# Optimization experiments

Measured on AMD Instinct MI355X. Metric: run time of the kernel, lower is better.

## Reference

```python
import jax, jax.numpy as jnp
import numpy as np

N = 100000
E = 1600000
NFEAT = 128
NHID = 128
NCLASS = 10


def setup_inputs() -> dict:
    key = jax.random.key(0)
    ks = jax.random.split(key, 12)
    x = jax.random.normal(ks[0], (N, NFEAT), dtype=jnp.float32)
    edge_index = jax.random.randint(ks[1], (2, E), 0, N, dtype=jnp.int64)
    s = 0.05
    W1 = jax.random.normal(ks[2], (NFEAT, NHID), dtype=jnp.float32) * s
    b1 = jnp.zeros((NHID,), dtype=jnp.float32)
    W2 = jax.random.normal(ks[3], (NHID, NHID), dtype=jnp.float32) * s
    b2 = jnp.zeros((NHID,), dtype=jnp.float32)
    W3 = jax.random.normal(ks[4], (NHID, NHID), dtype=jnp.float32) * s
    b3 = jnp.zeros((NHID,), dtype=jnp.float32)
    Wl = jax.random.normal(ks[5], (NHID, NCLASS), dtype=jnp.float32) * s
    bl = jnp.zeros((NCLASS,), dtype=jnp.float32)
    return {"x": x, "edge_index": edge_index, "W1": W1, "b1": b1,
            "W2": W2, "b2": b2, "W3": W3, "b3": b3, "Wl": Wl, "bl": bl}


def _gcn_norm(edge_index, num_nodes):
    # PyG gcn_norm with add_self_loops=True and unit edge weights.
    loops = jnp.arange(num_nodes, dtype=edge_index.dtype)
    src = jnp.concatenate([edge_index[0], loops])  # [E+N]
    dst = jnp.concatenate([edge_index[1], loops])
    ones = jnp.ones(src.shape[0], dtype=jnp.float32)
    deg = jax.ops.segment_sum(ones, dst, num_segments=num_nodes)
    dis = jax.lax.rsqrt(deg)  # deg >= 1 due to self-loops
    norm = dis[src] * dis[dst]  # [E+N]
    return src, dst, norm


def _gcn_conv(h, src, dst, norm, W, b, num_nodes):
    h = h @ W                                   # [N, out]
    msg = h[src] * norm[:, None]                # gather + edge scaling
    out = jax.ops.segment_sum(msg, dst, num_segments=num_nodes)
    return out + b


def reference(x, edge_index, W1, b1, W2, b2, W3, b3, Wl, bl):
    src, dst, norm = _gcn_norm(edge_index, N)
    h = jax.nn.relu(_gcn_conv(x, src, dst, norm, W1, b1, N))
    h = jax.nn.relu(_gcn_conv(h, src, dst, norm, W2, b2, N))
    h = _gcn_conv(h, src, dst, norm, W3, b3, N)
    logits = h @ Wl + bl                        # dropout is identity (eval / p=0)
    return jax.nn.log_softmax(logits, axis=1)
```

## Files before the change

### kernel.cpp

```cpp
#include <hip/hip_runtime.h>

#define NFEAT 128
#define NCLS  10
#define NCP   16
#define BROW  512
#define BINC  4096

static inline size_t alignup(size_t x) { return (x + 255) & ~size_t(255); }

__device__ __forceinline__ ushort f2bf(float f) {
  uint x = __float_as_uint(f);
  return (ushort)((x + 0x7fffu + ((x >> 16) & 1u)) >> 16);
}
__device__ __forceinline__ float bf2f(ushort u) {
  return __uint_as_float(((uint)u) << 16);
}

typedef short bf16x8 __attribute__((ext_vector_type(8)));
typedef float f32x4 __attribute__((ext_vector_type(4)));


__global__ void zero_ints(int* __restrict__ p, int n) {
  int i = blockIdx.x * 256 + threadIdx.x;
  if (i < n) p[i] = 0;
}

__global__ __launch_bounds__(256) void bucket_hist(const int* __restrict__ dst,
                                                   int* __restrict__ bkt_cnt,
                                                   int e, int nbkt) {
  __shared__ int hist[256];
  for (int t = threadIdx.x; t < nbkt; t += 256) hist[t] = 0;
  __syncthreads();
  int i = blockIdx.x * 256 + threadIdx.x;
  int stride = gridDim.x * 256;
  for (; i < e; i += stride) atomicAdd(&hist[dst[i] >> 9], 1);
  __syncthreads();
  for (int t = threadIdx.x; t < nbkt; t += 256)
    if (hist[t]) atomicAdd(&bkt_cnt[t], hist[t]);
}

__global__ __launch_bounds__(256) void bkt_scan(const int* __restrict__ bkt_cnt,
                                                int* __restrict__ bkt_off,
                                                int* __restrict__ gfrontier,
                                                int n, int nbkt) {
  __shared__ int sbuf[256];
  const int t = threadIdx.x;
  int x = 0;
  if (t < nbkt) {
    int lo = t << 9;
    int nodes = n - lo; if (nodes > BROW) nodes = BROW;
    x = bkt_cnt[t] + nodes;
  }
  sbuf[t] = x;
  __syncthreads();
  for (int off = 1; off < 256; off <<= 1) {
    int v = (t >= off) ? sbuf[t - off] : 0;
    __syncthreads();
    sbuf[t] += v;
    __syncthreads();
  }
  if (t < nbkt) { bkt_off[t] = sbuf[t] - x; gfrontier[t] = sbuf[t] - x; }
  if (t == nbkt - 1) bkt_off[nbkt] = sbuf[t];
}

__global__ __launch_bounds__(256) void bin_items(const int* __restrict__ ei,
                                                 int nE, int total, int nbkt,
                                                 int* __restrict__ gfrontier,
                                                 int2* __restrict__ binned) {
  __shared__ int hist[256];
  __shared__ int loff[256];
  __shared__ int gbase[256];
  __shared__ int sbuf[256];
  __shared__ int2 st[BINC];
  const int t = threadIdx.x;
  const int chunk0 = blockIdx.x * BINC;
  for (int q = t; q < nbkt; q += 256) hist[q] = 0;
  __syncthreads();
  for (int j = t; j < BINC; j += 256) {
    int i = chunk0 + j;
    if (i < total) {
      int d = (i < nE) ? ei[nE + i] : (i - nE);
      atomicAdd(&hist[d >> 9], 1);
    }
  }
  __syncthreads();
  int x = (t < nbkt) ? hist[t] : 0;
  sbuf[t] = x;
  __syncthreads();
  for (int off = 1; off < 256; off <<= 1) {
    int v = (t >= off) ? sbuf[t - off] : 0;
    __syncthreads();
    sbuf[t] += v;
    __syncthreads();
  }
  loff[t] = sbuf[t] - x;
  gbase[t] = (t < nbkt && x > 0) ? atomicAdd(&gfrontier[t], x) : 0;
  __syncthreads();
  hist[t] = loff[t];
  __syncthreads();
  for (int j = t; j < BINC; j += 256) {
    int i = chunk0 + j;
    if (i < total) {
      int s, d;
      if (i < nE) { s = ei[i]; d = ei[nE + i]; }
      else        { s = i - nE; d = s; }
      int p = atomicAdd(&hist[d >> 9], 1);
      st[p] = make_int2(s, d);
    }
  }
  __syncthreads();
  int M = total - chunk0; if (M > BINC) M = BINC;
  for (int j = t; j < M; j += 256) {
    int2 it = st[j];
    int b = it.y >> 9;
    binned[gbase[b] + (j - loff[b])] = it;
  }
}

__global__ __launch_bounds__(512) void bucket_finalize(const int2* __restrict__ binned,
                                                       const int* __restrict__ bkt_off,
                                                       int* __restrict__ row_ptr,
                                                       float* __restrict__ dis,
                                                       int* __restrict__ ev,
                                                       int n, int nbkt) {
  __shared__ int hist[BROW];
  __shared__ int sbuf[BROW];
  __shared__ int pre[BROW];
  __shared__ int front[BROW];
  const int b = blockIdx.x;
  const int t = threadIdx.x;
  const int row0 = b << 9;
  const int beg = bkt_off[b], end = bkt_off[b + 1];
  hist[t] = 0; front[t] = 0;
  __syncthreads();
  for (int j = beg + t; j < end; j += BROW)
    atomicAdd(&hist[binned[j].y - row0], 1);
  __syncthreads();
  const int x = hist[t];
  const int v = row0 + t;
  if (v < n) dis[v] = rsqrtf((float)x);
  sbuf[t] = x;
  __syncthreads();
  for (int off = 1; off < BROW; off <<= 1) {
    int val = (t >= off) ? sbuf[t - off] : 0;
    __syncthreads();
    sbuf[t] += val;
    __syncthreads();
  }
  pre[t] = sbuf[t] - x;
  if (v < n) row_ptr[v] = beg + pre[t];
  if (b == nbkt - 1 && t == 0) row_ptr[n] = end;
  __syncthreads();
  for (int j = beg + t; j < end; j += BROW) {
    int2 it = binned[j];
    int dl = it.y - row0;
    int slot = atomicAdd(&front[dl], 1);
    ev[beg + pre[dl] + slot] = it.x;
  }
}


__global__ __launch_bounds__(256) void fold_weights(const float* __restrict__ W3,
                                                    const float* __restrict__ Wl,
                                                    const float* __restrict__ b3,
                                                    const float* __restrict__ bl,
                                                    float* __restrict__ Wf,
                                                    float* __restrict__ bf) {
  int t = blockIdx.x * blockDim.x + threadIdx.x;
  if (t < NFEAT * NCP) {
    int r = t >> 4, c = t & 15;
    float s = 0.f;
    if (c < NCLS) {
      for (int k = 0; k < NFEAT; ++k) s += W3[r * NFEAT + k] * Wl[k * NCLS + c];
    }
    Wf[t] = s;
  }
  if (t < NCP) {
    float s = 0.f;
    if (t < NCLS) {
      s = bl[t];
      for (int k = 0; k < NFEAT; ++k) s += b3[k] * Wl[k * NCLS + t];
    }
    bf[t] = s;
  }
}

__global__ __launch_bounds__(256) void prep_w(const float* __restrict__ W,
                                              ushort* __restrict__ Wt) {
  int t = blockIdx.x * 256 + threadIdx.x;
  if (t < NFEAT * NFEAT) {
    int n = t >> 7, k = t & 127;
    Wt[n * NFEAT + k] = f2bf(W[k * NFEAT + n]);
  }
}


__global__ __launch_bounds__(256) void gemm_mfma(const float* __restrict__ A,
                                                 const ushort* __restrict__ Wt,
                                                 const float* __restrict__ dis,
                                                 ushort* __restrict__ Cb, int nrows) {
  __shared__ __align__(16) ushort As[64 * NFEAT];
  const int tid = threadIdx.x;
  const int row0 = blockIdx.x * 64;
  {
    const int m = tid >> 2;
    const int kc = (tid & 3) * 32;
    const int gr = row0 + m;
    float4 f[8];
    if (gr < nrows) {
      #pragma unroll
      for (int q = 0; q < 8; ++q)
        f[q] = *(const float4*)&A[(size_t)gr * NFEAT + kc + q * 4];
    } else {
      #pragma unroll
      for (int q = 0; q < 8; ++q) f[q] = make_float4(0.f, 0.f, 0.f, 0.f);
    }
    #pragma unroll
    for (int q = 0; q < 4; ++q) {
      union { ushort u[8]; int4 v; } pk;
      const float* fp = (const float*)&f[q * 2];
      #pragma unroll
      for (int j = 0; j < 8; ++j) pk.u[j] = f2bf(fp[j]);
      int byte = (m * 256 + (kc + q * 8) * 2) ^ ((m & 7) << 4);
      *(int4*)((char*)As + byte) = pk.v;
    }
  }
  __syncthreads();
  const int wave = tid >> 6;
  const int lane = tid & 63;
  const int m0 = wave * 16;
  bf16x8 afr[4];
  #pragma unroll
  for (int ks = 0; ks < 4; ++ks) {
    int m = m0 + (lane & 15);
    int kk = ks * 32 + (lane >> 4) * 8;
    int byte = (m * 256 + kk * 2) ^ ((m & 7) << 4);
    afr[ks] = *(const bf16x8*)((const char*)As + byte);
  }
  f32x4 acc[8];
  #pragma unroll
  for (int c = 0; c < 8; ++c) acc[c] = (f32x4){0.f, 0.f, 0.f, 0.f};
  #pragma unroll
  for (int c = 0; c < 8; ++c) {
    #pragma unroll
    for (int ks = 0; ks < 4; ++ks) {
      int n = c * 16 + (lane & 15);
      int kk = ks * 32 + (lane >> 4) * 8;
      bf16x8 bfr = *(const bf16x8*)&Wt[n * NFEAT + kk];
      acc[c] = __builtin_amdgcn_mfma_f32_16x16x32_bf16(afr[ks], bfr, acc[c], 0, 0, 0);
    }
  }
  const int gr_base = row0 + m0 + (lane >> 4) * 4;
  float dr[4];
  #pragma unroll
  for (int r = 0; r < 4; ++r)
    dr[r] = (gr_base + r < nrows) ? dis[gr_base + r] : 0.f;
  #pragma unroll
  for (int c = 0; c < 8; ++c) {
    #pragma unroll
    for (int r = 0; r < 4; ++r) {
      int gr = gr_base + r;
      if (gr < nrows)
        Cb[(size_t)gr * NFEAT + c * 16 + (lane & 15)] = f2bf(acc[c][r] * dr[r]);
    }
  }
}


__global__ __launch_bounds__(256) void aggregate(const ushort* __restrict__ hw,
                                                 const int* __restrict__ row_ptr,
                                                 const int* __restrict__ ev,
                                                 const float* __restrict__ dis,
                                                 const float* __restrict__ bias,
                                                 float* __restrict__ out,
                                                 int relu, int n) {
  const int wave = threadIdx.x >> 6;
  const int lane = threadIdx.x & 63;
  const int v = blockIdx.x * 4 + wave;
  if (v >= n) return;
  const int beg = row_ptr[v], end = row_ptr[v + 1];
  const int half = lane >> 5;
  const int hl = lane & 31;
  float4 acc = make_float4(0.f, 0.f, 0.f, 0.f);
  int e = beg + half;
  for (; e + 6 < end; e += 8) {
    int s0 = ev[e];
    int s1 = ev[e + 2];
    int s2 = ev[e + 4];
    int s3 = ev[e + 6];
    ushort4 q0 = *(const ushort4*)&hw[(size_t)s0 * NFEAT + hl * 4];
    ushort4 q1 = *(const ushort4*)&hw[(size_t)s1 * NFEAT + hl * 4];
    ushort4 q2 = *(const ushort4*)&hw[(size_t)s2 * NFEAT + hl * 4];
    ushort4 q3 = *(const ushort4*)&hw[(size_t)s3 * NFEAT + hl * 4];
    acc.x += bf2f(q0.x) + bf2f(q1.x) + bf2f(q2.x) + bf2f(q3.x);
    acc.y += bf2f(q0.y) + bf2f(q1.y) + bf2f(q2.y) + bf2f(q3.y);
    acc.z += bf2f(q0.z) + bf2f(q1.z) + bf2f(q2.z) + bf2f(q3.z);
    acc.w += bf2f(q0.w) + bf2f(q1.w) + bf2f(q2.w) + bf2f(q3.w);
  }
  for (; e < end; e += 2) {
    int s = ev[e];
    ushort4 q = *(const ushort4*)&hw[(size_t)s * NFEAT + hl * 4];
    acc.x += bf2f(q.x); acc.y += bf2f(q.y);
    acc.z += bf2f(q.z); acc.w += bf2f(q.w);
  }
  acc.x += __shfl_xor(acc.x, 32);
  acc.y += __shfl_xor(acc.y, 32);
  acc.z += __shfl_xor(acc.z, 32);
  acc.w += __shfl_xor(acc.w, 32);
  if (half == 0) {
    float dv = dis[v];
    float4 b = *(const float4*)&bias[hl * 4];
    acc.x = acc.x * dv + b.x; acc.y = acc.y * dv + b.y;
    acc.z = acc.z * dv + b.z; acc.w = acc.w * dv + b.w;
    if (relu) {
      acc.x = fmaxf(acc.x, 0.f); acc.y = fmaxf(acc.y, 0.f);
      acc.z = fmaxf(acc.z, 0.f); acc.w = fmaxf(acc.w, 0.f);
    }
    *(float4*)&out[(size_t)v * NFEAT + hl * 4] = acc;
  }
}


__global__ __launch_bounds__(256) void gemm_small(const float* __restrict__ A,
                                                  const float* __restrict__ Wf,
                                                  const float* __restrict__ dis,
                                                  float* __restrict__ G, int n) {
  __shared__ float Ws[NFEAT * NCP];
  for (int i = threadIdx.x; i < NFEAT * NCP; i += 256) Ws[i] = Wf[i];
  __syncthreads();
  const int v = blockIdx.x * 256 + threadIdx.x;
  if (v >= n) return;
  const float* Arow = A + (size_t)v * NFEAT;
  float acc[NCP];
  #pragma unroll
  for (int c = 0; c < NCP; ++c) acc[c] = 0.f;
  #pragma unroll 4
  for (int k = 0; k < NFEAT; k += 4) {
    float4 a = *(const float4*)&Arow[k];
    float av[4] = {a.x, a.y, a.z, a.w};
    #pragma unroll
    for (int j = 0; j < 4; ++j) {
      #pragma unroll
      for (int cq = 0; cq < NCP; cq += 4) {
        float4 w = *(const float4*)&Ws[(k + j) * NCP + cq];
        acc[cq + 0] += av[j] * w.x;
        acc[cq + 1] += av[j] * w.y;
        acc[cq + 2] += av[j] * w.z;
        acc[cq + 3] += av[j] * w.w;
      }
    }
  }
  const float dv = dis[v];
  #pragma unroll
  for (int cq = 0; cq < NCP; cq += 4)
    *(float4*)&G[(size_t)v * NCP + cq] =
        make_float4(acc[cq] * dv, acc[cq + 1] * dv, acc[cq + 2] * dv, acc[cq + 3] * dv);
}


__global__ __launch_bounds__(256) void agg_logits(const float* __restrict__ G,
                                                  const int* __restrict__ row_ptr,
                                                  const int* __restrict__ ev,
                                                  const float* __restrict__ dis,
                                                  const float* __restrict__ bf,
                                                  float* __restrict__ out, int n) {
  const int wave = threadIdx.x >> 6;
  const int lane = threadIdx.x & 63;
  const int v = blockIdx.x * 4 + wave;
  if (v >= n) return;
  const int beg = row_ptr[v], end = row_ptr[v + 1];
  const int g = lane >> 4;
  const int f = lane & 15;
  float acc = 0.f;
  int e = beg + g;
  for (; e + 4 < end; e += 8) {
    int s0 = ev[e];
    int s1 = ev[e + 4];
    acc += G[(size_t)s0 * NCP + f] + G[(size_t)s1 * NCP + f];
  }
  for (; e < end; e += 4) {
    acc += G[(size_t)ev[e] * NCP + f];
  }
  acc += __shfl_xor(acc, 16);
  acc += __shfl_xor(acc, 32);
  float logit = dis[v] * acc + bf[f];
  float pv = (f < NCLS) ? logit : -INFINITY;
  float m = pv;
  #pragma unroll
  for (int s = 8; s >= 1; s >>= 1) m = fmaxf(m, __shfl_xor(m, s));
  float ex = (f < NCLS) ? expf(logit - m) : 0.f;
  float ssum = ex;
  #pragma unroll
  for (int s = 8; s >= 1; s >>= 1) ssum += __shfl_xor(ssum, s);
  float lse = m + logf(ssum);
  if (g == 0 && f < NCLS) out[(size_t)v * NCLS + f] = logit - lse;
}


extern "C" void kernel_launch(void* const* d_in, const int* in_sizes, int n_in,
                              void* d_out, int out_size, void* d_ws, size_t ws_size,
                              hipStream_t stream) {
  const float* x  = (const float*)d_in[0];
  const int*   ei = (const int*)d_in[1];
  const float* W1 = (const float*)d_in[2];
  const float* b1 = (const float*)d_in[3];
  const float* W2 = (const float*)d_in[4];
  const float* b2 = (const float*)d_in[5];
  const float* W3 = (const float*)d_in[6];
  const float* b3 = (const float*)d_in[7];
  const float* Wl = (const float*)d_in[8];
  const float* bl = (const float*)d_in[9];
  float* out = (float*)d_out;

  const int nN = in_sizes[0] / NFEAT;
  const int nE = in_sizes[1] / 2;
  const int total = nN + nE;
  const int nbkt = (nN + BROW - 1) >> 9;
  const int nbBin = (total + BINC - 1) / BINC;

  char* ws = (char*)d_ws;
  int*    bkt_cnt = (int*)ws;     ws += alignup(256 * 4);
  int*    bkt_off = (int*)ws;     ws += alignup(257 * 4);
  int*    gfront  = (int*)ws;     ws += alignup(256 * 4);
  int*    row_ptr = (int*)ws;     ws += alignup((size_t)(nN + 1) * 4);
  float*  dis     = (float*)ws;   ws += alignup((size_t)nN * 4);
  float*  Wf      = (float*)ws;   ws += alignup((size_t)NFEAT * NCP * 4);
  float*  bf      = (float*)ws;   ws += alignup((size_t)NCP * 4);
  ushort* Wt1     = (ushort*)ws;  ws += alignup((size_t)NFEAT * NFEAT * 2);
  ushort* Wt2     = (ushort*)ws;  ws += alignup((size_t)NFEAT * NFEAT * 2);
  int2*   binned  = (int2*)ws;    ws += alignup((size_t)total * 8);
  int*    ev      = (int*)ws;     ws += alignup((size_t)total * 4);
  ushort* hb      = (ushort*)ws;  ws += alignup((size_t)nN * NFEAT * 2);
  float*  bufA    = (float*)ws;   ws += alignup((size_t)nN * NFEAT * 4);
  float*  G       = (float*)ws;   ws += alignup((size_t)nN * NCP * 4);

  zero_ints<<<1, 256, 0, stream>>>(bkt_cnt, nbkt);
  bucket_hist<<<512, 256, 0, stream>>>(ei + nE, bkt_cnt, nE, nbkt);
  bkt_scan<<<1, 256, 0, stream>>>(bkt_cnt, bkt_off, gfront, nN, nbkt);
  bin_items<<<nbBin, 256, 0, stream>>>(ei, nE, total, nbkt, gfront, binned);
  bucket_finalize<<<nbkt, BROW, 0, stream>>>(binned, bkt_off, row_ptr, dis, ev, nN, nbkt);

  fold_weights<<<8, 256, 0, stream>>>(W3, Wl, b3, bl, Wf, bf);
  prep_w<<<64, 256, 0, stream>>>(W1, Wt1);
  prep_w<<<64, 256, 0, stream>>>(W2, Wt2);

  const int gemm_grid = (nN + 63) / 64;
  const int node_grid = (nN + 3) / 4;

  gemm_mfma<<<gemm_grid, 256, 0, stream>>>(x, Wt1, dis, hb, nN);
  aggregate<<<node_grid, 256, 0, stream>>>(hb, row_ptr, ev, dis, b1, bufA, 1, nN);
  gemm_mfma<<<gemm_grid, 256, 0, stream>>>(bufA, Wt2, dis, hb, nN);
  aggregate<<<node_grid, 256, 0, stream>>>(hb, row_ptr, ev, dis, b2, bufA, 1, nN);
  gemm_small<<<(nN + 255) / 256, 256, 0, stream>>>(bufA, Wf, dis, G, nN);
  agg_logits<<<node_grid, 256, 0, stream>>>(G, row_ptr, ev, dis, bf, out, nN);
}
```

Baseline: 359.7 us.

## Store hidden features as feature-sliced bf16 planes to shrink gather working set

Hidden activations are stored as 8 planes of 16 features each (bf16) instead of row-major 128-wide rows. Each aggregate block works on one plane for 16 nodes, so the random gather touches a 3.2 MB plane that can stay cache-resident instead of the full feature matrix. Aggregate outputs are also written as bf16 planes rather than fp32, which halves the intermediate traffic feeding the next GEMM. The cost is that each edge list is re-read 8 times and each gathered access is only 8 bytes, and the GEMMs need plane-strided loads and stores.

```diff
diff --git a/kernel.cpp b/kernel.cpp
--- a/kernel.cpp
+++ b/kernel.cpp
@@ -195,34 +195,56 @@
 }
 
 
+template<bool SLICED>
 __global__ __launch_bounds__(256) void gemm_mfma(const float* __restrict__ A,
+                                                 const ushort* __restrict__ AS,
+                                                 size_t pstride,
                                                  const ushort* __restrict__ Wt,
                                                  const float* __restrict__ dis,
-                                                 ushort* __restrict__ Cb, int nrows) {
-  __shared__ __align__(16) ushort As[64 * NFEAT];
+                                                 ushort* __restrict__ CbS, int nrows) {
+  __shared__ __align__(16) ushort Asm[64 * NFEAT];
   const int tid = threadIdx.x;
   const int row0 = blockIdx.x * 64;
   {
     const int m = tid >> 2;
     const int kc = (tid & 3) * 32;
     const int gr = row0 + m;
-    float4 f[8];
-    if (gr < nrows) {
+    int4 u[4];
+    if (SLICED) {
+      if (gr < nrows) {
+        const int p0 = kc >> 4;
+        const ushort* pl0 = AS + (size_t)p0 * pstride + (size_t)gr * 16;
+        const ushort* pl1 = pl0 + pstride;
+        u[0] = *(const int4*)pl0;
+        u[1] = *(const int4*)(pl0 + 8);
+        u[2] = *(const int4*)pl1;
+        u[3] = *(const int4*)(pl1 + 8);
+      } else {
+        u[0] = u[1] = u[2] = u[3] = make_int4(0, 0, 0, 0);
+      }
+    } else {
+      float4 f[8];
+      if (gr < nrows) {
+        #pragma unroll
+        for (int q = 0; q < 8; ++q)
+          f[q] = *(const float4*)&A[(size_t)gr * NFEAT + kc + q * 4];
+      } else {
+        #pragma unroll
+        for (int q = 0; q < 8; ++q) f[q] = make_float4(0.f, 0.f, 0.f, 0.f);
+      }
       #pragma unroll
-      for (int q = 0; q < 8; ++q)
-        f[q] = *(const float4*)&A[(size_t)gr * NFEAT + kc + q * 4];
-    } else {
-      #pragma unroll
-      for (int q = 0; q < 8; ++q) f[q] = make_float4(0.f, 0.f, 0.f, 0.f);
+      for (int q = 0; q < 4; ++q) {
+        union { ushort us[8]; int4 v; } pk;
+        const float* fp = (const float*)&f[q * 2];
+        #pragma unroll
+        for (int j = 0; j < 8; ++j) pk.us[j] = f2bf(fp[j]);
+        u[q] = pk.v;
+      }
     }
     #pragma unroll
     for (int q = 0; q < 4; ++q) {
-      union { ushort u[8]; int4 v; } pk;
-      const float* fp = (const float*)&f[q * 2];
-      #pragma unroll
-      for (int j = 0; j < 8; ++j) pk.u[j] = f2bf(fp[j]);
       int byte = (m * 256 + (kc + q * 8) * 2) ^ ((m & 7) << 4);
-      *(int4*)((char*)As + byte) = pk.v;
+      *(int4*)((char*)Asm + byte) = u[q];
     }
   }
   __syncthreads();
@@ -235,7 +257,7 @@
     int m = m0 + (lane & 15);
     int kk = ks * 32 + (lane >> 4) * 8;
     int byte = (m * 256 + kk * 2) ^ ((m & 7) << 4);
-    afr[ks] = *(const bf16x8*)((const char*)As + byte);
+    afr[ks] = *(const bf16x8*)((const char*)Asm + byte);
   }
   f32x4 acc[8];
   #pragma unroll
@@ -257,71 +279,74 @@
     dr[r] = (gr_base + r < nrows) ? dis[gr_base + r] : 0.f;
   #pragma unroll
   for (int c = 0; c < 8; ++c) {
+    ushort* plane = CbS + (size_t)c * pstride;
     #pragma unroll
     for (int r = 0; r < 4; ++r) {
       int gr = gr_base + r;
       if (gr < nrows)
-        Cb[(size_t)gr * NFEAT + c * 16 + (lane & 15)] = f2bf(acc[c][r] * dr[r]);
-    }
-  }
-}
-
-
-__global__ __launch_bounds__(256) void aggregate(const ushort* __restrict__ hw,
+        plane[(size_t)gr * 16 + (lane & 15)] = f2bf(acc[c][r] * dr[r]);
+    }
+  }
+}
+
+
+__global__ __launch_bounds__(256) void aggregate(const ushort* __restrict__ hbS,
                                                  const int* __restrict__ row_ptr,
                                                  const int* __restrict__ ev,
                                                  const float* __restrict__ dis,
                                                  const float* __restrict__ bias,
-                                                 float* __restrict__ out,
-                                                 int relu, int n) {
+                                                 ushort* __restrict__ outS,
+                                                 size_t pstride, int relu, int n) {
+  const int s = blockIdx.x & 7;
+  const int chunk = blockIdx.x >> 3;
   const int wave = threadIdx.x >> 6;
   const int lane = threadIdx.x & 63;
-  const int v = blockIdx.x * 4 + wave;
-  if (v >= n) return;
-  const int beg = row_ptr[v], end = row_ptr[v + 1];
-  const int half = lane >> 5;
-  const int hl = lane & 31;
-  float4 acc = make_float4(0.f, 0.f, 0.f, 0.f);
-  int e = beg + half;
-  for (; e + 6 < end; e += 8) {
-    int s0 = ev[e];
-    int s1 = ev[e + 2];
-    int s2 = ev[e + 4];
-    int s3 = ev[e + 6];
-    ushort4 q0 = *(const ushort4*)&hw[(size_t)s0 * NFEAT + hl * 4];
-    ushort4 q1 = *(const ushort4*)&hw[(size_t)s1 * NFEAT + hl * 4];
-    ushort4 q2 = *(const ushort4*)&hw[(size_t)s2 * NFEAT + hl * 4];
-    ushort4 q3 = *(const ushort4*)&hw[(size_t)s3 * NFEAT + hl * 4];
-    acc.x += bf2f(q0.x) + bf2f(q1.x) + bf2f(q2.x) + bf2f(q3.x);
-    acc.y += bf2f(q0.y) + bf2f(q1.y) + bf2f(q2.y) + bf2f(q3.y);
-    acc.z += bf2f(q0.z) + bf2f(q1.z) + bf2f(q2.z) + bf2f(q3.z);
-    acc.w += bf2f(q0.w) + bf2f(q1.w) + bf2f(q2.w) + bf2f(q3.w);
-  }
-  for (; e < end; e += 2) {
-    int s = ev[e];
-    ushort4 q = *(const ushort4*)&hw[(size_t)s * NFEAT + hl * 4];
-    acc.x += bf2f(q.x); acc.y += bf2f(q.y);
-    acc.z += bf2f(q.z); acc.w += bf2f(q.w);
-  }
-  acc.x += __shfl_xor(acc.x, 32);
-  acc.y += __shfl_xor(acc.y, 32);
-  acc.z += __shfl_xor(acc.z, 32);
-  acc.w += __shfl_xor(acc.w, 32);
-  if (half == 0) {
-    float dv = dis[v];
-    float4 b = *(const float4*)&bias[hl * 4];
-    acc.x = acc.x * dv + b.x; acc.y = acc.y * dv + b.y;
-    acc.z = acc.z * dv + b.z; acc.w = acc.w * dv + b.w;
-    if (relu) {
-      acc.x = fmaxf(acc.x, 0.f); acc.y = fmaxf(acc.y, 0.f);
-      acc.z = fmaxf(acc.z, 0.f); acc.w = fmaxf(acc.w, 0.f);
-    }
-    *(float4*)&out[(size_t)v * NFEAT + hl * 4] = acc;
-  }
-}
-
-
-__global__ __launch_bounds__(256) void gemm_small(const float* __restrict__ A,
+  const int f4 = lane & 3;
+  const int ep = lane >> 2;
+  const ushort* plane = hbS + (size_t)s * pstride;
+  ushort* oplane = outS + (size_t)s * pstride;
+  const float4 bs = *(const float4*)&bias[s * 16 + f4 * 4];
+  #pragma unroll
+  for (int q = 0; q < 4; ++q) {
+    const int v = chunk * 16 + wave * 4 + q;
+    if (v >= n) return;
+    const int beg = row_ptr[v], end = row_ptr[v + 1];
+    float4 acc = make_float4(0.f, 0.f, 0.f, 0.f);
+    for (int e = beg + ep; e < end; e += 16) {
+      int src = __builtin_nontemporal_load(&ev[e]);
+      ushort4 q4 = *(const ushort4*)&plane[(size_t)src * 16 + f4 * 4];
+      acc.x += bf2f(q4.x); acc.y += bf2f(q4.y);
+      acc.z += bf2f(q4.z); acc.w += bf2f(q4.w);
+    }
+    #pragma unroll
+    for (int off = 4; off <= 32; off <<= 1) {
+      acc.x += __shfl_xor(acc.x, off);
+      acc.y += __shfl_xor(acc.y, off);
+      acc.z += __shfl_xor(acc.z, off);
+      acc.w += __shfl_xor(acc.w, off);
+    }
+    if (ep == 0) {
+      const float dv = dis[v];
+      float4 r;
+      r.x = fmaf(acc.x, dv, bs.x);
+      r.y = fmaf(acc.y, dv, bs.y);
+      r.z = fmaf(acc.z, dv, bs.z);
+      r.w = fmaf(acc.w, dv, bs.w);
+      if (relu) {
+        r.x = fmaxf(r.x, 0.f); r.y = fmaxf(r.y, 0.f);
+        r.z = fmaxf(r.z, 0.f); r.w = fmaxf(r.w, 0.f);
+      }
+      union { ushort us[4]; uint2 q2; } pk;
+      pk.us[0] = f2bf(r.x); pk.us[1] = f2bf(r.y);
+      pk.us[2] = f2bf(r.z); pk.us[3] = f2bf(r.w);
+      *(uint2*)&oplane[(size_t)v * 16 + f4 * 4] = pk.q2;
+    }
+  }
+}
+
+
+__global__ __launch_bounds__(256) void gemm_small(const ushort* __restrict__ AS,
+                                                  size_t pstride,
                                                   const float* __restrict__ Wf,
                                                   const float* __restrict__ dis,
                                                   float* __restrict__ G, int n) {
@@ -330,23 +355,26 @@
   __syncthreads();
   const int v = blockIdx.x * 256 + threadIdx.x;
   if (v >= n) return;
-  const float* Arow = A + (size_t)v * NFEAT;
   float acc[NCP];
   #pragma unroll
   for (int c = 0; c < NCP; ++c) acc[c] = 0.f;
-  #pragma unroll 4
-  for (int k = 0; k < NFEAT; k += 4) {
-    float4 a = *(const float4*)&Arow[k];
-    float av[4] = {a.x, a.y, a.z, a.w};
+  #pragma unroll
+  for (int p = 0; p < 8; ++p) {
+    union { ushort us[16]; int4 q[2]; } a;
+    const ushort* pl = AS + (size_t)p * pstride + (size_t)v * 16;
+    a.q[0] = *(const int4*)pl;
+    a.q[1] = *(const int4*)(pl + 8);
     #pragma unroll
-    for (int j = 0; j < 4; ++j) {
+    for (int j = 0; j < 16; ++j) {
+      float av = bf2f(a.us[j]);
+      int k = p * 16 + j;
       #pragma unroll
       for (int cq = 0; cq < NCP; cq += 4) {
-        float4 w = *(const float4*)&Ws[(k + j) * NCP + cq];
-        acc[cq + 0] += av[j] * w.x;
-        acc[cq + 1] += av[j] * w.y;
-        acc[cq + 2] += av[j] * w.z;
-        acc[cq + 3] += av[j] * w.w;
+        float4 w = *(const float4*)&Ws[k * NCP + cq];
+        acc[cq + 0] += av * w.x;
+        acc[cq + 1] += av * w.y;
+        acc[cq + 2] += av * w.z;
+        acc[cq + 3] += av * w.w;
       }
     }
   }
@@ -417,6 +445,7 @@
   const int total = nN + nE;
   const int nbkt = (nN + BROW - 1) >> 9;
   const int nbBin = (total + BINC - 1) / BINC;
+  const size_t pstride = (size_t)nN * 16;
 
   char* ws = (char*)d_ws;
   int*    bkt_cnt = (int*)ws;     ws += alignup(256 * 4);
@@ -425,13 +454,13 @@
   int*    row_ptr = (int*)ws;     ws += alignup((size_t)(nN + 1) * 4);
   float*  dis     = (float*)ws;   ws += alignup((size_t)nN * 4);
   float*  Wf      = (float*)ws;   ws += alignup((size_t)NFEAT * NCP * 4);
-  float*  bf      = (float*)ws;   ws += alignup((size_t)NCP * 4);
+  float*  bfv     = (float*)ws;   ws += alignup((size_t)NCP * 4);
   ushort* Wt1     = (ushort*)ws;  ws += alignup((size_t)NFEAT * NFEAT * 2);
   ushort* Wt2     = (ushort*)ws;  ws += alignup((size_t)NFEAT * NFEAT * 2);
   int2*   binned  = (int2*)ws;    ws += alignup((size_t)total * 8);
   int*    ev      = (int*)ws;     ws += alignup((size_t)total * 4);
-  ushort* hb      = (ushort*)ws;  ws += alignup((size_t)nN * NFEAT * 2);
-  float*  bufA    = (float*)ws;   ws += alignup((size_t)nN * NFEAT * 4);
+  ushort* hbS     = (ushort*)ws;  ws += alignup((size_t)nN * NFEAT * 2);
+  ushort* aggS    = (ushort*)ws;  ws += alignup((size_t)nN * NFEAT * 2);
   float*  G       = (float*)ws;   ws += alignup((size_t)nN * NCP * 4);
 
   zero_ints<<<1, 256, 0, stream>>>(bkt_cnt, nbkt);
@@ -440,17 +469,18 @@
   bin_items<<<nbBin, 256, 0, stream>>>(ei, nE, total, nbkt, gfront, binned);
   bucket_finalize<<<nbkt, BROW, 0, stream>>>(binned, bkt_off, row_ptr, dis, ev, nN, nbkt);
 
-  fold_weights<<<8, 256, 0, stream>>>(W3, Wl, b3, bl, Wf, bf);
+  fold_weights<<<8, 256, 0, stream>>>(W3, Wl, b3, bl, Wf, bfv);
   prep_w<<<64, 256, 0, stream>>>(W1, Wt1);
   prep_w<<<64, 256, 0, stream>>>(W2, Wt2);
 
   const int gemm_grid = (nN + 63) / 64;
+  const int agg_grid = ((nN + 15) / 16) * 8;
   const int node_grid = (nN + 3) / 4;
 
-  gemm_mfma<<<gemm_grid, 256, 0, stream>>>(x, Wt1, dis, hb, nN);
-  aggregate<<<node_grid, 256, 0, stream>>>(hb, row_ptr, ev, dis, b1, bufA, 1, nN);
-  gemm_mfma<<<gemm_grid, 256, 0, stream>>>(bufA, Wt2, dis, hb, nN);
-  aggregate<<<node_grid, 256, 0, stream>>>(hb, row_ptr, ev, dis, b2, bufA, 1, nN);
-  gemm_small<<<(nN + 255) / 256, 256, 0, stream>>>(bufA, Wf, dis, G, nN);
-  agg_logits<<<node_grid, 256, 0, stream>>>(G, row_ptr, ev, dis, bf, out, nN);
-}
+  gemm_mfma<false><<<gemm_grid, 256, 0, stream>>>(x, nullptr, pstride, Wt1, dis, hbS, nN);
+  aggregate<<<agg_grid, 256, 0, stream>>>(hbS, row_ptr, ev, dis, b1, aggS, pstride, 1, nN);
+  gemm_mfma<true><<<gemm_grid, 256, 0, stream>>>(nullptr, aggS, pstride, Wt2, dis, hbS, nN);
+  aggregate<<<agg_grid, 256, 0, stream>>>(hbS, row_ptr, ev, dis, b2, aggS, pstride, 1, nN);
+  gemm_small<<<(nN + 255) / 256, 256, 0, stream>>>(aggS, pstride, Wf, dis, G, nN);
+  agg_logits<<<node_grid, 256, 0, stream>>>(G, row_ptr, ev, dis, bfv, out, nN);
+}
```

Measured after the change: 710.6 us. 1.98x slower.

## Fuse aggregation with following GEMM via shared-memory tile and bf16 intermediates

Applied to the files above, without the earlier changes.

Each aggregation step now writes its ReLU'd 64-row tile into shared memory as bf16 and immediately runs the next MFMA GEMM, so the fp32 intermediate buffer is never written to or re-read from global memory. The folded W3·Wl projection now runs on MFMA with a single 16-column tile, and the logits intermediate G is stored as bf16. Small launches are also merged: a memset replaces the zero kernel and the two weight preps become one kernel. The risks are lower occupancy, since each block aggregates 16 nodes per wave serially before the GEMM, and extra bf16 rounding of intermediates.

```diff
diff --git a/kernel.cpp b/kernel.cpp
--- a/kernel.cpp
+++ b/kernel.cpp
@@ -19,11 +19,6 @@
 typedef short bf16x8 __attribute__((ext_vector_type(8)));
 typedef float f32x4 __attribute__((ext_vector_type(4)));
 
-
-__global__ void zero_ints(int* __restrict__ p, int n) {
-  int i = blockIdx.x * 256 + threadIdx.x;
-  if (i < n) p[i] = 0;
-}
 
 __global__ __launch_bounds__(256) void bucket_hist(const int* __restrict__ dst,
                                                    int* __restrict__ bkt_cnt,
@@ -164,7 +159,7 @@
                                                     const float* __restrict__ Wl,
                                                     const float* __restrict__ b3,
                                                     const float* __restrict__ bl,
-                                                    float* __restrict__ Wf,
+                                                    ushort* __restrict__ Wft,
                                                     float* __restrict__ bf) {
   int t = blockIdx.x * blockDim.x + threadIdx.x;
   if (t < NFEAT * NCP) {
@@ -173,7 +168,7 @@
     if (c < NCLS) {
       for (int k = 0; k < NFEAT; ++k) s += W3[r * NFEAT + k] * Wl[k * NCLS + c];
     }
-    Wf[t] = s;
+    Wft[c * NFEAT + r] = f2bf(s);
   }
   if (t < NCP) {
     float s = 0.f;
@@ -185,13 +180,15 @@
   }
 }
 
-__global__ __launch_bounds__(256) void prep_w(const float* __restrict__ W,
-                                              ushort* __restrict__ Wt) {
+__global__ __launch_bounds__(256) void prep_w2(const float* __restrict__ W1,
+                                               const float* __restrict__ W2,
+                                               ushort* __restrict__ Wt1,
+                                               ushort* __restrict__ Wt2) {
   int t = blockIdx.x * 256 + threadIdx.x;
-  if (t < NFEAT * NFEAT) {
-    int n = t >> 7, k = t & 127;
-    Wt[n * NFEAT + k] = f2bf(W[k * NFEAT + n]);
-  }
+  int u = t & 16383;
+  int n = u >> 7, k = u & 127;
+  if (t < 16384) Wt1[n * NFEAT + k] = f2bf(W1[k * NFEAT + n]);
+  else           Wt2[n * NFEAT + k] = f2bf(W2[k * NFEAT + n]);
 }
 
 
@@ -199,7 +196,7 @@
                                                  const ushort* __restrict__ Wt,
                                                  const float* __restrict__ dis,
                                                  ushort* __restrict__ Cb, int nrows) {
-  __shared__ __align__(16) ushort As[64 * NFEAT];
+  __shared__ __align__(16) ushort Asm[64 * NFEAT];
   const int tid = threadIdx.x;
   const int row0 = blockIdx.x * 64;
   {
@@ -217,12 +214,12 @@
     }
     #pragma unroll
     for (int q = 0; q < 4; ++q) {
-      union { ushort u[8]; int4 v; } pk;
+      union { ushort us[8]; int4 v; } pk;
       const float* fp = (const float*)&f[q * 2];
       #pragma unroll
-      for (int j = 0; j < 8; ++j) pk.u[j] = f2bf(fp[j]);
+      for (int j = 0; j < 8; ++j) pk.us[j] = f2bf(fp[j]);
       int byte = (m * 256 + (kc + q * 8) * 2) ^ ((m & 7) << 4);
-      *(int4*)((char*)As + byte) = pk.v;
+      *(int4*)((char*)Asm + byte) = pk.v;
     }
   }
   __syncthreads();
@@ -235,7 +232,7 @@
     int m = m0 + (lane & 15);
     int kk = ks * 32 + (lane >> 4) * 8;
     int byte = (m * 256 + kk * 2) ^ ((m & 7) << 4);
-    afr[ks] = *(const bf16x8*)((const char*)As + byte);
+    afr[ks] = *(const bf16x8*)((const char*)Asm + byte);
   }
   f32x4 acc[8];
   #pragma unroll
@@ -267,98 +264,111 @@
 }
 
 
-__global__ __launch_bounds__(256) void aggregate(const ushort* __restrict__ hw,
-                                                 const int* __restrict__ row_ptr,
-                                                 const int* __restrict__ ev,
-                                                 const float* __restrict__ dis,
-                                                 const float* __restrict__ bias,
-                                                 float* __restrict__ out,
-                                                 int relu, int n) {
-  const int wave = threadIdx.x >> 6;
-  const int lane = threadIdx.x & 63;
-  const int v = blockIdx.x * 4 + wave;
-  if (v >= n) return;
-  const int beg = row_ptr[v], end = row_ptr[v + 1];
+template<int NCT>
+__global__ __launch_bounds__(256) void fused_agg_gemm(const ushort* __restrict__ hw,
+                                                      const int* __restrict__ row_ptr,
+                                                      const int* __restrict__ ev,
+                                                      const float* __restrict__ dis,
+                                                      const float* __restrict__ bias,
+                                                      const ushort* __restrict__ Wt,
+                                                      ushort* __restrict__ outB, int n) {
+  __shared__ __align__(16) ushort Hs[64 * NFEAT];
+  const int tid = threadIdx.x;
+  const int wave = tid >> 6;
+  const int lane = tid & 63;
   const int half = lane >> 5;
   const int hl = lane & 31;
-  float4 acc = make_float4(0.f, 0.f, 0.f, 0.f);
-  int e = beg + half;
-  for (; e + 6 < end; e += 8) {
-    int s0 = ev[e];
-    int s1 = ev[e + 2];
-    int s2 = ev[e + 4];
-    int s3 = ev[e + 6];
-    ushort4 q0 = *(const ushort4*)&hw[(size_t)s0 * NFEAT + hl * 4];
-    ushort4 q1 = *(const ushort4*)&hw[(size_t)s1 * NFEAT + hl * 4];
-    ushort4 q2 = *(const ushort4*)&hw[(size_t)s2 * NFEAT + hl * 4];
-    ushort4 q3 = *(const ushort4*)&hw[(size_t)s3 * NFEAT + hl * 4];
-    acc.x += bf2f(q0.x) + bf2f(q1.x) + bf2f(q2.x) + bf2f(q3.x);
-    acc.y += bf2f(q0.y) + bf2f(q1.y) + bf2f(q2.y) + bf2f(q3.y);
-    acc.z += bf2f(q0.z) + bf2f(q1.z) + bf2f(q2.z) + bf2f(q3.z);
-    acc.w += bf2f(q0.w) + bf2f(q1.w) + bf2f(q2.w) + bf2f(q3.w);
-  }
-  for (; e < end; e += 2) {
-    int s = ev[e];
-    ushort4 q = *(const ushort4*)&hw[(size_t)s * NFEAT + hl * 4];
-    acc.x += bf2f(q.x); acc.y += bf2f(q.y);
-    acc.z += bf2f(q.z); acc.w += bf2f(q.w);
-  }
-  acc.x += __shfl_xor(acc.x, 32);
-  acc.y += __shfl_xor(acc.y, 32);
-  acc.z += __shfl_xor(acc.z, 32);
-  acc.w += __shfl_xor(acc.w, 32);
-  if (half == 0) {
-    float dv = dis[v];
-    float4 b = *(const float4*)&bias[hl * 4];
-    acc.x = acc.x * dv + b.x; acc.y = acc.y * dv + b.y;
-    acc.z = acc.z * dv + b.z; acc.w = acc.w * dv + b.w;
-    if (relu) {
-      acc.x = fmaxf(acc.x, 0.f); acc.y = fmaxf(acc.y, 0.f);
-      acc.z = fmaxf(acc.z, 0.f); acc.w = fmaxf(acc.w, 0.f);
-    }
-    *(float4*)&out[(size_t)v * NFEAT + hl * 4] = acc;
-  }
-}
-
-
-__global__ __launch_bounds__(256) void gemm_small(const float* __restrict__ A,
-                                                  const float* __restrict__ Wf,
-                                                  const float* __restrict__ dis,
-                                                  float* __restrict__ G, int n) {
-  __shared__ float Ws[NFEAT * NCP];
-  for (int i = threadIdx.x; i < NFEAT * NCP; i += 256) Ws[i] = Wf[i];
-  __syncthreads();
-  const int v = blockIdx.x * 256 + threadIdx.x;
-  if (v >= n) return;
-  const float* Arow = A + (size_t)v * NFEAT;
-  float acc[NCP];
-  #pragma unroll
-  for (int c = 0; c < NCP; ++c) acc[c] = 0.f;
-  #pragma unroll 4
-  for (int k = 0; k < NFEAT; k += 4) {
-    float4 a = *(const float4*)&Arow[k];
-    float av[4] = {a.x, a.y, a.z, a.w};
+  const int row0 = blockIdx.x * 64;
+  const float4 bs = *(const float4*)&bias[hl * 4];
+  for (int q = 0; q < 16; ++q) {
+    const int m = wave * 16 + q;
+    const int v = row0 + m;
+    float4 acc = make_float4(0.f, 0.f, 0.f, 0.f);
+    if (v < n) {
+      const int beg = row_ptr[v], end = row_ptr[v + 1];
+      int e = beg + half;
+      for (; e + 6 < end; e += 8) {
+        int s0 = ev[e];
+        int s1 = ev[e + 2];
+        int s2 = ev[e + 4];
+        int s3 = ev[e + 6];
+        ushort4 q0 = *(const ushort4*)&hw[(size_t)s0 * NFEAT + hl * 4];
+        ushort4 q1 = *(const ushort4*)&hw[(size_t)s1 * NFEAT + hl * 4];
+        ushort4 q2 = *(const ushort4*)&hw[(size_t)s2 * NFEAT + hl * 4];
+        ushort4 q3 = *(const ushort4*)&hw[(size_t)s3 * NFEAT + hl * 4];
+        acc.x += bf2f(q0.x) + bf2f(q1.x) + bf2f(q2.x) + bf2f(q3.x);
+        acc.y += bf2f(q0.y) + bf2f(q1.y) + bf2f(q2.y) + bf2f(q3.y);
+        acc.z += bf2f(q0.z) + bf2f(q1.z) + bf2f(q2.z) + bf2f(q3.z);
+        acc.w += bf2f(q0.w) + bf2f(q1.w) + bf2f(q2.w) + bf2f(q3.w);
+      }
+      for (; e < end; e += 2) {
+        int s = ev[e];
+        ushort4 q4 = *(const ushort4*)&hw[(size_t)s * NFEAT + hl * 4];
+        acc.x += bf2f(q4.x); acc.y += bf2f(q4.y);
+        acc.z += bf2f(q4.z); acc.w += bf2f(q4.w);
+      }
+      acc.x += __shfl_xor(acc.x, 32);
+      acc.y += __shfl_xor(acc.y, 32);
+      acc.z += __shfl_xor(acc.z, 32);
+      acc.w += __shfl_xor(acc.w, 32);
+    }
+    if (half == 0) {
+      float r0 = 0.f, r1 = 0.f, r2 = 0.f, r3 = 0.f;
+      if (v < n) {
+        const float dv = dis[v];
+        r0 = fmaxf(fmaf(acc.x, dv, bs.x), 0.f);
+        r1 = fmaxf(fmaf(acc.y, dv, bs.y), 0.f);
+        r2 = fmaxf(fmaf(acc.z, dv, bs.z), 0.f);
+        r3 = fmaxf(fmaf(acc.w, dv, bs.w), 0.f);
+      }
+      union { ushort us[4]; uint2 q2; } pk;
+      pk.us[0] = f2bf(r0); pk.us[1] = f2bf(r1);
+      pk.us[2] = f2bf(r2); pk.us[3] = f2bf(r3);
+      int byte = (m * 256 + hl * 8) ^ ((m & 7) << 4);
+      *(uint2*)((char*)Hs + byte) = pk.q2;
+    }
+  }
+  __syncthreads();
+  const int m0 = wave * 16;
+  bf16x8 afr[4];
+  #pragma unroll
+  for (int ks = 0; ks < 4; ++ks) {
+    int m = m0 + (lane & 15);
+    int kk = ks * 32 + (lane >> 4) * 8;
+    int byte = (m * 256 + kk * 2) ^ ((m & 7) << 4);
+    afr[ks] = *(const bf16x8*)((const char*)Hs + byte);
+  }
+  f32x4 acc[NCT];
+  #pragma unroll
+  for (int c = 0; c < NCT; ++c) acc[c] = (f32x4){0.f, 0.f, 0.f, 0.f};
+  #pragma unroll
+  for (int c = 0; c < NCT; ++c) {
     #pragma unroll
-    for (int j = 0; j < 4; ++j) {
-      #pragma unroll
-      for (int cq = 0; cq < NCP; cq += 4) {
-        float4 w = *(const float4*)&Ws[(k + j) * NCP + cq];
-        acc[cq + 0] += av[j] * w.x;
-        acc[cq + 1] += av[j] * w.y;
-        acc[cq + 2] += av[j] * w.z;
-        acc[cq + 3] += av[j] * w.w;
-      }
-    }
-  }
-  const float dv = dis[v];
-  #pragma unroll
-  for (int cq = 0; cq < NCP; cq += 4)
-    *(float4*)&G[(size_t)v * NCP + cq] =
-        make_float4(acc[cq] * dv, acc[cq + 1] * dv, acc[cq + 2] * dv, acc[cq + 3] * dv);
-}
-
-
-__global__ __launch_bounds__(256) void agg_logits(const float* __restrict__ G,
+    for (int ks = 0; ks < 4; ++ks) {
+      int nn = c * 16 + (lane & 15);
+      int kk = ks * 32 + (lane >> 4) * 8;
+      bf16x8 bfr = *(const bf16x8*)&Wt[nn * NFEAT + kk];
+      acc[c] = __builtin_amdgcn_mfma_f32_16x16x32_bf16(afr[ks], bfr, acc[c], 0, 0, 0);
+    }
+  }
+  const int gr_base = row0 + m0 + (lane >> 4) * 4;
+  float dr[4];
+  #pragma unroll
+  for (int r = 0; r < 4; ++r)
+    dr[r] = (gr_base + r < n) ? dis[gr_base + r] : 0.f;
+  #pragma unroll
+  for (int c = 0; c < NCT; ++c) {
+    #pragma unroll
+    for (int r = 0; r < 4; ++r) {
+      int gr = gr_base + r;
+      if (gr < n)
+        outB[(size_t)gr * (NCT * 16) + c * 16 + (lane & 15)] = f2bf(acc[c][r] * dr[r]);
+    }
+  }
+}
+
+
+__global__ __launch_bounds__(256) void agg_logits(const ushort* __restrict__ Gb,
                                                   const int* __restrict__ row_ptr,
                                                   const int* __restrict__ ev,
                                                   const float* __restrict__ dis,
@@ -376,10 +386,10 @@
   for (; e + 4 < end; e += 8) {
     int s0 = ev[e];
     int s1 = ev[e + 4];
-    acc += G[(size_t)s0 * NCP + f] + G[(size_t)s1 * NCP + f];
+    acc += bf2f(Gb[(size_t)s0 * NCP + f]) + bf2f(Gb[(size_t)s1 * NCP + f]);
   }
   for (; e < end; e += 4) {
-    acc += G[(size_t)ev[e] * NCP + f];
+    acc += bf2f(Gb[(size_t)ev[e] * NCP + f]);
   }
   acc += __shfl_xor(acc, 16);
   acc += __shfl_xor(acc, 32);
@@ -424,33 +434,30 @@
   int*    gfront  = (int*)ws;     ws += alignup(256 * 4);
   int*    row_ptr = (int*)ws;     ws += alignup((size_t)(nN + 1) * 4);
   float*  dis     = (float*)ws;   ws += alignup((size_t)nN * 4);
-  float*  Wf      = (float*)ws;   ws += alignup((size_t)NFEAT * NCP * 4);
-  float*  bf      = (float*)ws;   ws += alignup((size_t)NCP * 4);
+  float*  bfv     = (float*)ws;   ws += alignup((size_t)NCP * 4);
+  ushort* Wft     = (ushort*)ws;  ws += alignup((size_t)NCP * NFEAT * 2);
   ushort* Wt1     = (ushort*)ws;  ws += alignup((size_t)NFEAT * NFEAT * 2);
   ushort* Wt2     = (ushort*)ws;  ws += alignup((size_t)NFEAT * NFEAT * 2);
   int2*   binned  = (int2*)ws;    ws += alignup((size_t)total * 8);
   int*    ev      = (int*)ws;     ws += alignup((size_t)total * 4);
   ushort* hb      = (ushort*)ws;  ws += alignup((size_t)nN * NFEAT * 2);
-  float*  bufA    = (float*)ws;   ws += alignup((size_t)nN * NFEAT * 4);
-  float*  G       = (float*)ws;   ws += alignup((size_t)nN * NCP * 4);
-
-  zero_ints<<<1, 256, 0, stream>>>(bkt_cnt, nbkt);
+  ushort* hb2     = (ushort*)ws;  ws += alignup((size_t)nN * NFEAT * 2);
+  ushort* Gb      = (ushort*)ws;  ws += alignup((size_t)nN * NCP * 2);
+
+  hipMemsetAsync(bkt_cnt, 0, 256 * sizeof(int), stream);
   bucket_hist<<<512, 256, 0, stream>>>(ei + nE, bkt_cnt, nE, nbkt);
   bkt_scan<<<1, 256, 0, stream>>>(bkt_cnt, bkt_off, gfront, nN, nbkt);
   bin_items<<<nbBin, 256, 0, stream>>>(ei, nE, total, nbkt, gfront, binned);
   bucket_finalize<<<nbkt, BROW, 0, stream>>>(binned, bkt_off, row_ptr, dis, ev, nN, nbkt);
 
-  fold_weights<<<8, 256, 0, stream>>>(W3, Wl, b3, bl, Wf, bf);
-  prep_w<<<64, 256, 0, stream>>>(W1, Wt1);
-  prep_w<<<64, 256, 0, stream>>>(W2, Wt2);
+  fold_weights<<<8, 256, 0, stream>>>(W3, Wl, b3, bl, Wft, bfv);
+  prep_w2<<<128, 256, 0, stream>>>(W1, W2, Wt1, Wt2);
 
   const int gemm_grid = (nN + 63) / 64;
   const int node_grid = (nN + 3) / 4;
 
   gemm_mfma<<<gemm_grid, 256, 0, stream>>>(x, Wt1, dis, hb, nN);
-  aggregate<<<node_grid, 256, 0, stream>>>(hb, row_ptr, ev, dis, b1, bufA, 1, nN);
-  gemm_mfma<<<gemm_grid, 256, 0, stream>>>(bufA, Wt2, dis, hb, nN);
-  aggregate<<<node_grid, 256, 0, stream>>>(hb, row_ptr, ev, dis, b2, bufA, 1, nN);
-  gemm_small<<<(nN + 255) / 256, 256, 0, stream>>>(bufA, Wf, dis, G, nN);
-  agg_logits<<<node_grid, 256, 0, stream>>>(G, row_ptr, ev, dis, bf, out, nN);
-}
+  fused_agg_gemm<8><<<gemm_grid, 256, 0, stream>>>(hb, row_ptr, ev, dis, b1, Wt2, hb2, nN);
+  fused_agg_gemm<1><<<gemm_grid, 256, 0, stream>>>(hb2, row_ptr, ev, dis, b2, Wft, Gb, nN);
+  agg_logits<<<node_grid, 256, 0, stream>>>(Gb, row_ptr, ev, dis, bfv, out, nN);
+}
```

Result: slower. 387.3 us (+7.7%).
